# Kernel optimization log

Hardware: AMD Instinct MI355X
Metric: run time of the kernel (lower is better)

## Reference

```python
import jax, jax.numpy as jnp
import numpy as np

EPS_WSUM = 1e-12
EPS_NORM = 1e-12


def setup_inputs() -> dict:
    key = jax.random.key(0)
    ks = jax.random.split(key, 8)
    N, E, D = 100000, 800000, 128
    x = jax.random.normal(ks[0], (N, D), dtype=jnp.float32)
    edge_index = jax.random.randint(ks[1], (2, E), 0, N, dtype=jnp.int64)
    edge_weight = jax.random.uniform(ks[2], (E,), dtype=jnp.float32)
    # Linear(in_dim*2, out_dim): weight [out, 2*in], bias [out]
    W1 = jax.random.normal(ks[3], (D, 2 * D), dtype=jnp.float32) * (1.0 / np.sqrt(2 * D))
    b1 = jnp.zeros((D,), dtype=jnp.float32)
    W2 = jax.random.normal(ks[4], (D, 2 * D), dtype=jnp.float32) * (1.0 / np.sqrt(2 * D))
    b2 = jnp.zeros((D,), dtype=jnp.float32)
    return {"x": x, "edge_index": edge_index, "edge_weight": edge_weight,
            "W1": W1, "b1": b1, "W2": W2, "b2": b2}


def _weighted_neighbor_mean(x, src, dst, w):
    # messages: gather neighbor features at dst, weight per-edge  [E, D]
    msgs = x[dst] * w[:, None]
    num_nodes = x.shape[0]
    agg = jax.ops.segment_sum(msgs, src, num_segments=num_nodes)   # [N, D]
    wsum = jax.ops.segment_sum(w, src, num_segments=num_nodes)     # [N]
    return agg / jnp.maximum(wsum, EPS_WSUM)[:, None]


def _sage_layer(x, src, dst, w, W, b):
    neigh = _weighted_neighbor_mean(x, src, dst, w)
    h = jnp.concatenate([x, neigh], axis=1)          # [N, 2D]
    h = h @ W.T + b                                   # [N, D]
    return jax.nn.relu(h)


def reference(x, edge_index, edge_weight, W1, b1, W2, b2):
    src = edge_index[0]
    dst = edge_index[1]
    h = _sage_layer(x, src, dst, edge_weight, W1, b1)
    h = _sage_layer(h, src, dst, edge_weight, W2, b2)
    # F.normalize(dim=1): x / max(||x||_2, eps)
    norm = jnp.linalg.norm(h, axis=1, keepdims=True)
    return h / jnp.maximum(norm, EPS_NORM)
```

## Files before the change

kernel.cpp:

```cpp
#include <hip/hip_runtime.h>
#include <hip/hip_bf16.h>

#define D 128
#define BSH 8
#define BMASK 255

typedef __attribute__((ext_vector_type(8))) short bf16x8;
typedef __attribute__((ext_vector_type(4))) float f32x4;
typedef unsigned short u16;
typedef unsigned int u32;

__device__ inline u16 f2bf(float f) {
    union { float f; u32 u; } v; v.f = f;
    u32 r = v.u + 0x7FFFu + ((v.u >> 16) & 1u);
    return (u16)(r >> 16);
}

__global__ void cast3_kernel(const float* __restrict__ a, const float* __restrict__ b,
                             const float* __restrict__ c, u16* __restrict__ oa,
                             u16* __restrict__ ob, u16* __restrict__ oc,
                             int na4, int nw4,
                             int* __restrict__ bCursor, int nbuk, int cap) {
    int i = blockIdx.x * blockDim.x + threadIdx.x;
    if (i < nbuk) bCursor[i] = i * cap;
    const float* in; u16* out; int k;
    if (i < na4)                { in = a; out = oa; k = i; }
    else if (i < na4 + nw4)     { in = b; out = ob; k = i - na4; }
    else if (i < na4 + 2 * nw4) { in = c; out = oc; k = i - na4 - nw4; }
    else return;
    float4 v = *(const float4*)(in + (size_t)k * 4);
    u32 lo = (u32)f2bf(v.x) | ((u32)f2bf(v.y) << 16);
    u32 hi = (u32)f2bf(v.z) | ((u32)f2bf(v.w) << 16);
    *(uint2*)(out + (size_t)k * 4) = make_uint2(lo, hi);
}

__global__ void partition_kernel(const int* __restrict__ src, const int* __restrict__ dst,
                                 const float* __restrict__ w, int* __restrict__ bucketCursor,
                                 uint2* __restrict__ temp, int E, int nbuk) {
    __shared__ int cnt[1024];
    __shared__ int base[1024];
    int per = (E + gridDim.x - 1) / gridDim.x;
    int lo = blockIdx.x * per;
    int hi = min(E, lo + per);
    for (int i = threadIdx.x; i < nbuk; i += blockDim.x) cnt[i] = 0;
    __syncthreads();
    for (int i = lo + threadIdx.x; i < hi; i += blockDim.x)
        atomicAdd(&cnt[src[i] >> BSH], 1);
    __syncthreads();
    for (int i = threadIdx.x; i < nbuk; i += blockDim.x)
        base[i] = cnt[i] ? atomicAdd(&bucketCursor[i], cnt[i]) : 0;
    __syncthreads();
    for (int i = threadIdx.x; i < nbuk; i += blockDim.x) cnt[i] = 0;
    __syncthreads();
    for (int i = lo + threadIdx.x; i < hi; i += blockDim.x) {
        int s = src[i];
        int b = s >> BSH;
        int off = atomicAdd(&cnt[b], 1);
        temp[base[b] + off] =
            make_uint2((u32)dst[i] | ((u32)(s & BMASK) << 17), __float_as_uint(w[i]));
    }
}

__global__ void bucket_csr(const uint2* __restrict__ temp, const int* __restrict__ bucketEnd,
                           uint2* __restrict__ rowse, uint2* __restrict__ edge,
                           int N, int cap) {
    int b = blockIdx.x;
    int lo = b * cap;
    int hi = bucketEnd[b];
    int t = threadIdx.x;
    __shared__ int deg_l[256];
    __shared__ int sc[256];
    __shared__ int cur[256];
    deg_l[t] = 0;
    __syncthreads();
    for (int i = lo + t; i < hi; i += 256)
        atomicAdd(&deg_l[temp[i].x >> 17], 1);
    __syncthreads();
    int mydeg = deg_l[t];
    sc[t] = mydeg;
    __syncthreads();
    for (int off = 1; off < 256; off <<= 1) {
        int v = (t >= off) ? sc[t - off] : 0;
        __syncthreads();
        sc[t] += v;
        __syncthreads();
    }
    int excl = (t == 0) ? 0 : sc[t - 1];
    int gnode = (b << BSH) + t;
    if (gnode < N) rowse[gnode] = make_uint2((u32)(lo + excl), (u32)mydeg);
    cur[t] = excl;
    __syncthreads();
    for (int i = lo + t; i < hi; i += 256) {
        uint2 r = temp[i];
        int p = atomicAdd(&cur[r.x >> 17], 1);
        edge[lo + p] = make_uint2(r.x & 0x1FFFFu, r.y);
    }
}

__global__ void aggregate_kernel(const u16* __restrict__ feat,
                                 const uint2* __restrict__ rowse,
                                 const uint2* __restrict__ edge,
                                 u16* __restrict__ neigh, int n) {
    const char* fb = (const char*)feat;
    int wv = blockIdx.x * 4 + (threadIdx.x >> 6);
    int lane = threadIdx.x & 63;
    int node0 = wv * 2;
    if (node0 >= n) return;
    const u32 lo4 = (u32)lane * 4u;
    int nend = min(node0 + 2, n);
    for (int node = node0; node < nend; ++node) {
        uint2 se = rowse[node];
        int beg = __builtin_amdgcn_readfirstlane((int)se.x);
        int deg = __builtin_amdgcn_readfirstlane((int)se.y);
        int end = beg + deg;
        float ax = 0.f, ay = 0.f, ws = 0.f;
        int j = beg;
        for (; j + 3 < end; j += 4) {
            uint2 e0 = edge[j], e1 = edge[j + 1], e2 = edge[j + 2], e3 = edge[j + 3];
            float w0 = __uint_as_float(e0.y), w1 = __uint_as_float(e1.y);
            float w2 = __uint_as_float(e2.y), w3 = __uint_as_float(e3.y);
            u32 u0 = *(const u32*)(fb + e0.x * 256u + lo4);
            u32 u1 = *(const u32*)(fb + e1.x * 256u + lo4);
            u32 u2 = *(const u32*)(fb + e2.x * 256u + lo4);
            u32 u3 = *(const u32*)(fb + e3.x * 256u + lo4);
            ax += __uint_as_float(u0 << 16) * w0 + __uint_as_float(u1 << 16) * w1
                + __uint_as_float(u2 << 16) * w2 + __uint_as_float(u3 << 16) * w3;
            ay += __uint_as_float(u0 & 0xFFFF0000u) * w0 + __uint_as_float(u1 & 0xFFFF0000u) * w1
                + __uint_as_float(u2 & 0xFFFF0000u) * w2 + __uint_as_float(u3 & 0xFFFF0000u) * w3;
            ws += w0 + w1 + w2 + w3;
        }
        for (; j < end; ++j) {
            uint2 e0 = edge[j];
            float w0 = __uint_as_float(e0.y);
            u32 u0 = *(const u32*)(fb + e0.x * 256u + lo4);
            ax += __uint_as_float(u0 << 16) * w0;
            ay += __uint_as_float(u0 & 0xFFFF0000u) * w0;
            ws += w0;
        }
        float inv = 1.0f / fmaxf(ws, 1e-12f);
        u32 o = (u32)f2bf(ax * inv) | ((u32)f2bf(ay * inv) << 16);
        *(u32*)(neigh + (size_t)node * D + lane * 2) = o;
    }
}

template <bool NORM>
__global__ void __launch_bounds__(512, 2)
sage_gemm(const u16* __restrict__ axb,
          const u16* __restrict__ aneigh,
          const u16* __restrict__ Wb,
          const float* __restrict__ bias,
          u16* __restrict__ outB,
          float* __restrict__ outF,
          int n) {
    __shared__ __attribute__((aligned(16))) char smem[65536];

    const int tid  = threadIdx.x;
    const int wave = tid >> 6;
    const int lane = tid & 63;
    const int quad = lane >> 4;
    const int l16  = lane & 15;
    const int r0   = blockIdx.x * 256 + wave * 32;

    bf16x8 a[2][8];
    {
        int ra = r0 + l16;        if (ra >= n) ra = n - 1;
        int rb = r0 + 16 + l16;   if (rb >= n) rb = n - 1;
        const u16* p00 = axb    + (size_t)ra * D + quad * 8;
        const u16* p10 = axb    + (size_t)rb * D + quad * 8;
        const u16* p01 = aneigh + (size_t)ra * D + quad * 8;
        const u16* p11 = aneigh + (size_t)rb * D + quad * 8;
#pragma unroll
        for (int kk = 0; kk < 4; ++kk) {
            a[0][kk] = *(const bf16x8*)(p00 + kk * 32);
            a[1][kk] = *(const bf16x8*)(p10 + kk * 32);
        }
#pragma unroll
        for (int kk = 0; kk < 4; ++kk) {
            a[0][4 + kk] = *(const bf16x8*)(p01 + kk * 32);
            a[1][4 + kk] = *(const bf16x8*)(p11 + kk * 32);
        }
    }

#pragma unroll
    for (int it = 0; it < 8; ++it) {
        int e = it * 512 + tid;
        int c  = e >> 5;
        int kc = e & 31;
        uint4 v = *(const uint4*)(Wb + (size_t)c * 256 + kc * 8);
        u32 off = (((u32)c << 9) + ((u32)kc << 4)) ^ (((u32)c & 7u) << 4);
        *(uint4*)(smem + off) = v;
    }
    __syncthreads();

    f32x4 acc[2][8];
#pragma unroll
    for (int s = 0; s < 2; ++s)
#pragma unroll
        for (int c = 0; c < 8; ++c)
            acc[s][c] = (f32x4){0.f, 0.f, 0.f, 0.f};

#pragma unroll
    for (int kk = 0; kk < 8; ++kk) {
#pragma unroll
        for (int c = 0; c < 8; ++c) {
            u32 col = (u32)(c * 16 + l16);
            u32 off = ((col << 9) + ((u32)(kk * 4 + quad) << 4)) ^ ((col & 7u) << 4);
            bf16x8 b = *(const bf16x8*)(smem + off);
            acc[0][c] = __builtin_amdgcn_mfma_f32_16x16x32_bf16(a[0][kk], b, acc[0][c], 0, 0, 0);
            acc[1][c] = __builtin_amdgcn_mfma_f32_16x16x32_bf16(a[1][kk], b, acc[1][c], 0, 0, 0);
        }
    }

    __syncthreads();

    float bvals[8];
#pragma unroll
    for (int c = 0; c < 8; ++c) bvals[c] = bias[c * 16 + l16];

    if (NORM) {
        float* stg = (float*)smem + wave * 2048;
#pragma unroll
        for (int s = 0; s < 2; ++s) {
#pragma unroll
            for (int reg = 0; reg < 4; ++reg) {
                float v[8];
#pragma unroll
                for (int c = 0; c < 8; ++c)
                    v[c] = fmaxf(acc[s][c][reg] + bvals[c], 0.0f);
                float ss = 0.f;
#pragma unroll
                for (int c = 0; c < 8; ++c) ss += v[c] * v[c];
                ss += __shfl_xor(ss, 1);
                ss += __shfl_xor(ss, 2);
                ss += __shfl_xor(ss, 4);
                ss += __shfl_xor(ss, 8);
                float inv = 1.0f / fmaxf(sqrtf(ss), 1e-12f);
#pragma unroll
                for (int c = 0; c < 8; ++c)
                    stg[(quad * 4 + reg) * 128 + c * 16 + l16] = v[c] * inv;
            }
#pragma unroll
            for (int p = 0; p < 8; ++p) {
                int lr = 2 * p + (lane >> 5);
                int grow = r0 + s * 16 + lr;
                float4 val = *(float4*)&stg[lr * 128 + (lane & 31) * 4];
                if (grow < n)
                    *(float4*)(outF + (size_t)grow * D + (lane & 31) * 4) = val;
            }
        }
    } else {
        u16* stg = (u16*)smem + wave * 2048;
#pragma unroll
        for (int s = 0; s < 2; ++s) {
#pragma unroll
            for (int reg = 0; reg < 4; ++reg) {
#pragma unroll
                for (int c = 0; c < 8; ++c) {
                    float v = fmaxf(acc[s][c][reg] + bvals[c], 0.0f);
                    stg[(quad * 4 + reg) * 128 + c * 16 + l16] = f2bf(v);
                }
            }
#pragma unroll
            for (int p = 0; p < 4; ++p) {
                int lr = 4 * p + (lane >> 4);
                int grow = r0 + s * 16 + lr;
                uint4 val = *(uint4*)&stg[lr * 128 + l16 * 8];
                if (grow < n)
                    *(uint4*)(outB + (size_t)grow * D + l16 * 8) = val;
            }
        }
    }
}

extern "C" void kernel_launch(void* const* d_in, const int* in_sizes, int n_in,
                              void* d_out, int out_size, void* d_ws, size_t ws_size,
                              hipStream_t stream) {
    const float* x  = (const float*)d_in[0];
    const int*   ei = (const int*)d_in[1];
    const float* ew = (const float*)d_in[2];
    const float* W1 = (const float*)d_in[3];
    const float* b1 = (const float*)d_in[4];
    const float* W2 = (const float*)d_in[5];
    const float* b2 = (const float*)d_in[6];
    float* out = (float*)d_out;

    const int E = in_sizes[2];
    const int N = in_sizes[0] / D;
    const int nbuk = (N + BMASK) >> BSH;
    const int CAP = ((2 * (E / nbuk + 1) + 1023) / 1024) * 1024;

    const int* src = ei;
    const int* dst = ei + E;

    char* p = (char*)d_ws;
    auto alloc = [&](size_t bytes) { char* r = p; p += (bytes + 255) & ~(size_t)255; return r; };
    u16*   xb      = (u16*)  alloc((size_t)N * D * sizeof(u16));
    u16*   hB      = (u16*)  alloc((size_t)N * D * sizeof(u16));
    u16*   neighB  = (u16*)  alloc((size_t)N * D * sizeof(u16));
    uint2* temp    = (uint2*)alloc(((size_t)nbuk * CAP + 64) * 8);
    uint2* edge    = (uint2*)alloc(((size_t)nbuk * CAP + 64) * 8);
    u16*   Wb1     = (u16*)  alloc((size_t)D * 2 * D * sizeof(u16));
    u16*   Wb2     = (u16*)  alloc((size_t)D * 2 * D * sizeof(u16));
    uint2* rowse   = (uint2*)alloc((size_t)N * sizeof(uint2));
    int*   bCursor = (int*)  alloc((size_t)(nbuk + 1) * sizeof(int));

    const int gemmGrid = (N + 255) / 256;
    const int n4 = N * D / 4;
    const int w4 = D * 2 * D / 4;
    const int castTotal = n4 + 2 * w4;
    const int aggGrid = ((N + 1) / 2 + 3) / 4;

    cast3_kernel    <<<(castTotal + 255) / 256, 256, 0, stream>>>(x, W1, W2, xb, Wb1, Wb2,
                                                                  n4, w4, bCursor, nbuk, CAP);
    partition_kernel<<<256, 256, 0, stream>>>(src, dst, ew, bCursor, temp, E, nbuk);
    bucket_csr      <<<nbuk, 256, 0, stream>>>(temp, bCursor, rowse, edge, N, CAP);

    aggregate_kernel<<<aggGrid, 256, 0, stream>>>(xb, rowse, edge, neighB, N);
    sage_gemm<false><<<gemmGrid, 512, 0, stream>>>(xb, neighB, Wb1, b1, hB, nullptr, N);

    aggregate_kernel<<<aggGrid, 256, 0, stream>>>(hB, rowse, edge, neighB, N);
    sage_gemm<true><<<gemmGrid, 512, 0, stream>>>(hB, neighB, Wb2, b2, nullptr, out, N);
}
```

Before: 261.2 us.

## Split aggregate wave into four 16-lane groups with 16-byte row gathers

The neighbor aggregation kernel now has each wave handle four nodes instead of two. Within a wave, the 64 lanes split into four 16-lane groups that each gather a different edge's 256-byte bf16 row using 16-byte loads, covering eight edges per iteration. Partial sums are combined across the groups with cross-lane shuffles, and the first group writes the result with one 16-byte store. This trades narrow per-lane loads for wider ones and more independent gathers in flight, at the cost of shuffle reductions, clamped tail edges that do wasted loads, and lower wave-level parallelism.

```diff
diff --git a/kernel.cpp b/kernel.cpp
--- a/kernel.cpp
+++ b/kernel.cpp
@@ -102,44 +102,67 @@
                                  const uint2* __restrict__ edge,
                                  u16* __restrict__ neigh, int n) {
     const char* fb = (const char*)feat;
-    int wv = blockIdx.x * 4 + (threadIdx.x >> 6);
+    int wv   = blockIdx.x * 4 + (threadIdx.x >> 6);
     int lane = threadIdx.x & 63;
-    int node0 = wv * 2;
+    int grp  = lane >> 4;
+    int l16  = lane & 15;
+    int node0 = wv * 4;
     if (node0 >= n) return;
-    const u32 lo4 = (u32)lane * 4u;
-    int nend = min(node0 + 2, n);
-    for (int node = node0; node < nend; ++node) {
-        uint2 se = rowse[node];
-        int beg = __builtin_amdgcn_readfirstlane((int)se.x);
-        int deg = __builtin_amdgcn_readfirstlane((int)se.y);
-        int end = beg + deg;
-        float ax = 0.f, ay = 0.f, ws = 0.f;
-        int j = beg;
-        for (; j + 3 < end; j += 4) {
-            uint2 e0 = edge[j], e1 = edge[j + 1], e2 = edge[j + 2], e3 = edge[j + 3];
-            float w0 = __uint_as_float(e0.y), w1 = __uint_as_float(e1.y);
-            float w2 = __uint_as_float(e2.y), w3 = __uint_as_float(e3.y);
-            u32 u0 = *(const u32*)(fb + e0.x * 256u + lo4);
-            u32 u1 = *(const u32*)(fb + e1.x * 256u + lo4);
-            u32 u2 = *(const u32*)(fb + e2.x * 256u + lo4);
-            u32 u3 = *(const u32*)(fb + e3.x * 256u + lo4);
-            ax += __uint_as_float(u0 << 16) * w0 + __uint_as_float(u1 << 16) * w1
-                + __uint_as_float(u2 << 16) * w2 + __uint_as_float(u3 << 16) * w3;
-            ay += __uint_as_float(u0 & 0xFFFF0000u) * w0 + __uint_as_float(u1 & 0xFFFF0000u) * w1
-                + __uint_as_float(u2 & 0xFFFF0000u) * w2 + __uint_as_float(u3 & 0xFFFF0000u) * w3;
-            ws += w0 + w1 + w2 + w3;
-        }
-        for (; j < end; ++j) {
-            uint2 e0 = edge[j];
-            float w0 = __uint_as_float(e0.y);
-            u32 u0 = *(const u32*)(fb + e0.x * 256u + lo4);
-            ax += __uint_as_float(u0 << 16) * w0;
-            ay += __uint_as_float(u0 & 0xFFFF0000u) * w0;
-            ws += w0;
-        }
+
+    int begs[4], degs[4];
+#pragma unroll
+    for (int i = 0; i < 4; ++i) {
+        int nd = node0 + i; if (nd > n - 1) nd = n - 1;
+        uint2 se = rowse[nd];
+        begs[i] = __builtin_amdgcn_readfirstlane((int)se.x);
+        degs[i] = __builtin_amdgcn_readfirstlane((int)se.y);
+    }
+
+#pragma unroll 1
+    for (int i = 0; i < 4; ++i) {
+        int node = node0 + i;
+        if (node >= n) break;
+        int beg = begs[i];
+        int end = beg + degs[i];
+        float acc[8] = {0.f, 0.f, 0.f, 0.f, 0.f, 0.f, 0.f, 0.f};
+        float ws = 0.f;
+        for (int j = beg; j < end; j += 8) {
+            int ia = j + grp;
+            int ib = j + 4 + grp;
+            int ca = ia < end ? ia : end - 1;
+            int cb = ib < end ? ib : end - 1;
+            uint2 ea = edge[ca];
+            uint2 eb = edge[cb];
+            float wa = (ia < end) ? __uint_as_float(ea.y) : 0.f;
+            float wb = (ib < end) ? __uint_as_float(eb.y) : 0.f;
+            uint4 ua = *(const uint4*)(fb + (size_t)ea.x * 256u + (u32)l16 * 16u);
+            uint4 ub = *(const uint4*)(fb + (size_t)eb.x * 256u + (u32)l16 * 16u);
+            u32 va[4] = {ua.x, ua.y, ua.z, ua.w};
+            u32 vb[4] = {ub.x, ub.y, ub.z, ub.w};
+#pragma unroll
+            for (int kk = 0; kk < 4; ++kk) {
+                acc[kk * 2]     += __uint_as_float(va[kk] << 16) * wa
+                                 + __uint_as_float(vb[kk] << 16) * wb;
+                acc[kk * 2 + 1] += __uint_as_float(va[kk] & 0xFFFF0000u) * wa
+                                 + __uint_as_float(vb[kk] & 0xFFFF0000u) * wb;
+            }
+            ws += wa + wb;
+        }
+#pragma unroll
+        for (int kk = 0; kk < 8; ++kk) {
+            acc[kk] += __shfl_xor(acc[kk], 16);
+            acc[kk] += __shfl_xor(acc[kk], 32);
+        }
+        ws += __shfl_xor(ws, 16);
+        ws += __shfl_xor(ws, 32);
         float inv = 1.0f / fmaxf(ws, 1e-12f);
-        u32 o = (u32)f2bf(ax * inv) | ((u32)f2bf(ay * inv) << 16);
-        *(u32*)(neigh + (size_t)node * D + lane * 2) = o;
+        if (grp == 0) {
+            u32 o0 = (u32)f2bf(acc[0] * inv) | ((u32)f2bf(acc[1] * inv) << 16);
+            u32 o1 = (u32)f2bf(acc[2] * inv) | ((u32)f2bf(acc[3] * inv) << 16);
+            u32 o2 = (u32)f2bf(acc[4] * inv) | ((u32)f2bf(acc[5] * inv) << 16);
+            u32 o3 = (u32)f2bf(acc[6] * inv) | ((u32)f2bf(acc[7] * inv) << 16);
+            *(uint4*)(neigh + (size_t)node * D + l16 * 8) = make_uint4(o0, o1, o2, o3);
+        }
     }
 }
 
@@ -308,7 +331,7 @@
     const int n4 = N * D / 4;
     const int w4 = D * 2 * D / 4;
     const int castTotal = n4 + 2 * w4;
-    const int aggGrid = ((N + 1) / 2 + 3) / 4;
+    const int aggGrid = (N + 15) / 16;
 
     cast3_kernel    <<<(castTotal + 255) / 256, 256, 0, stream>>>(x, W1, W2, xb, Wb1, Wb2,
                                                                   n4, w4, bCursor, nbuk, CAP);
```

Measured after the change: 263.7 us. No clear change (+1.0%).
